# Kernel tuning notes

Hardware: AMD Instinct MI355X
Metric: run time of the kernel (lower is better)

Reference implementation:

```python
import jax, jax.numpy as jnp
import numpy as np


def setup_inputs() -> dict:
    key = jax.random.key(0)
    k1, k2 = jax.random.split(key)
    embed1 = jax.random.normal(k1, (4096, 32), dtype=jnp.float32)
    embed2 = jax.random.normal(k2, (4096, 32), dtype=jnp.float32)
    return {"embed1": embed1, "embed2": embed2}


def reference(embed1, embed2):
    # Chebyshev (L-inf) pairwise distance matrix: [N, M]
    # diff: [N, M, D] broadcasted subtract, abs, max over feature dim D
    return jnp.max(jnp.abs(embed1[:, None, :] - embed2[None, :, :]), axis=2)
```

## Files before the change

### kernel.cpp

```cpp
#include <hip/hip_runtime.h>

#define FD 32
#define TILE 64
#define LSTRIDE (TILE + 4)

__global__ __launch_bounds__(256) void cheb_kernel(
    const float* __restrict__ A, const float* __restrict__ B,
    float* __restrict__ C, int N, int M)
{
    __shared__ float sA[FD][LSTRIDE];
    __shared__ float sB[FD][LSTRIDE];

    const int tid = threadIdx.x;
    const int r0 = blockIdx.y * TILE;
    const int c0 = blockIdx.x * TILE;

#pragma unroll
    for (int k = 0; k < 2; ++k) {
        const int idx = tid + k * 256;
        const int row = idx >> 3;
        const int dq  = (idx & 7) * 4;
        const float4 va = *reinterpret_cast<const float4*>(A + (size_t)(r0 + row) * FD + dq);
        sA[dq + 0][row] = va.x;
        sA[dq + 1][row] = va.y;
        sA[dq + 2][row] = va.z;
        sA[dq + 3][row] = va.w;
        const float4 vb = *reinterpret_cast<const float4*>(B + (size_t)(c0 + row) * FD + dq);
        sB[dq + 0][row] = vb.x;
        sB[dq + 1][row] = vb.y;
        sB[dq + 2][row] = vb.z;
        sB[dq + 3][row] = vb.w;
    }
    __syncthreads();

    const int tx = tid & 15;
    const int ty = tid >> 4;

    float acc[4][4];
#pragma unroll
    for (int i = 0; i < 4; ++i)
#pragma unroll
        for (int j = 0; j < 4; ++j)
            acc[i][j] = 0.0f;

#pragma unroll
    for (int d = 0; d < FD; ++d) {
        const float4 a4 = *reinterpret_cast<const float4*>(&sA[d][ty * 4]);
        const float4 b4 = *reinterpret_cast<const float4*>(&sB[d][tx * 4]);
        const float a[4] = {a4.x, a4.y, a4.z, a4.w};
        const float b[4] = {b4.x, b4.y, b4.z, b4.w};
#pragma unroll
        for (int i = 0; i < 4; ++i)
#pragma unroll
            for (int j = 0; j < 4; ++j)
                acc[i][j] = fmaxf(acc[i][j], fabsf(a[i] - b[j]));
    }

#pragma unroll
    for (int i = 0; i < 4; ++i) {
        const int row = r0 + ty * 4 + i;
        float4 o;
        o.x = acc[i][0]; o.y = acc[i][1]; o.z = acc[i][2]; o.w = acc[i][3];
        *reinterpret_cast<float4*>(C + (size_t)row * M + c0 + tx * 4) = o;
    }
}

extern "C" void kernel_launch(void* const* d_in, const int* in_sizes, int n_in,
                              void* d_out, int out_size, void* d_ws, size_t ws_size,
                              hipStream_t stream) {
    const float* A = (const float*)d_in[0];
    const float* B = (const float*)d_in[1];
    float* C = (float*)d_out;
    const int N = in_sizes[0] / FD;
    const int M = in_sizes[1] / FD;
    dim3 grid(M / TILE, N / TILE);
    cheb_kernel<<<grid, 256, 0, stream>>>(A, B, C, N, M);
}
```

Before: 25.15 us.

## Use 128x128 tiles with 8x8 per-thread outputs, packed subtract and max3-abs

The block tile grows from 64x64 to 128x128, and each thread now computes an 8x8 block of outputs. Shared memory holds B negated in a paired-dimension layout with an XOR swizzle, so v_pk_add_f32 computes two dimension differences per instruction. v_max3_f32 with abs modifiers then folds both into the running max, roughly halving the VALU instruction count per output. The cost is much higher register pressure (64 accumulators plus operands) and a grid reduced to 1024 blocks, which may lower occupancy.

Measured after the change: 34.76 us. +38.2%, slower.

```diff
diff --git a/kernel.cpp b/kernel.cpp
--- a/kernel.cpp
+++ b/kernel.cpp
@@ -1,67 +1,102 @@
 #include <hip/hip_runtime.h>
 
 #define FD 32
-#define TILE 64
-#define LSTRIDE (TILE + 4)
+#define NDD 16
+#define TILE 128
+#define PLANE 260
+
+__device__ __forceinline__ float2 pk_add(float2 a, float2 b) {
+    float2 r;
+    asm("v_pk_add_f32 %0, %1, %2" : "=v"(r) : "v"(a), "v"(b));
+    return r;
+}
+__device__ __forceinline__ float max3abs(float a, float x, float y) {
+    float r;
+    asm("v_max3_f32 %0, %1, abs(%2), abs(%3)" : "=v"(r) : "v"(a), "v"(x), "v"(y));
+    return r;
+}
 
 __global__ __launch_bounds__(256) void cheb_kernel(
     const float* __restrict__ A, const float* __restrict__ B,
-    float* __restrict__ C, int N, int M)
+    float* __restrict__ C, int M)
 {
-    __shared__ float sA[FD][LSTRIDE];
-    __shared__ float sB[FD][LSTRIDE];
+    __shared__ __align__(16) float sA[NDD * PLANE];
+    __shared__ __align__(16) float sB[NDD * PLANE];
 
     const int tid = threadIdx.x;
     const int r0 = blockIdx.y * TILE;
     const int c0 = blockIdx.x * TILE;
 
 #pragma unroll
-    for (int k = 0; k < 2; ++k) {
+    for (int k = 0; k < 4; ++k) {
         const int idx = tid + k * 256;
         const int row = idx >> 3;
         const int dq  = (idx & 7) * 4;
+        const int c   = row >> 1;
+        const int pc  = c ^ (c >> 3);
+        const int base = (dq >> 1) * PLANE + pc * 4 + (row & 1) * 2;
         const float4 va = *reinterpret_cast<const float4*>(A + (size_t)(r0 + row) * FD + dq);
-        sA[dq + 0][row] = va.x;
-        sA[dq + 1][row] = va.y;
-        sA[dq + 2][row] = va.z;
-        sA[dq + 3][row] = va.w;
+        sA[base + 0] = va.x;  sA[base + 1] = va.y;
+        sA[base + PLANE + 0] = va.z;  sA[base + PLANE + 1] = va.w;
         const float4 vb = *reinterpret_cast<const float4*>(B + (size_t)(c0 + row) * FD + dq);
-        sB[dq + 0][row] = vb.x;
-        sB[dq + 1][row] = vb.y;
-        sB[dq + 2][row] = vb.z;
-        sB[dq + 3][row] = vb.w;
+        sB[base + 0] = -vb.x;  sB[base + 1] = -vb.y;
+        sB[base + PLANE + 0] = -vb.z;  sB[base + PLANE + 1] = -vb.w;
     }
     __syncthreads();
 
     const int tx = tid & 15;
     const int ty = tid >> 4;
 
-    float acc[4][4];
+    float acc[8][8];
 #pragma unroll
-    for (int i = 0; i < 4; ++i)
+    for (int i = 0; i < 8; ++i)
 #pragma unroll
-        for (int j = 0; j < 4; ++j)
+        for (int j = 0; j < 8; ++j)
             acc[i][j] = 0.0f;
 
+    int swA[4], swB[4];
 #pragma unroll
-    for (int d = 0; d < FD; ++d) {
-        const float4 a4 = *reinterpret_cast<const float4*>(&sA[d][ty * 4]);
-        const float4 b4 = *reinterpret_cast<const float4*>(&sB[d][tx * 4]);
-        const float a[4] = {a4.x, a4.y, a4.z, a4.w};
-        const float b[4] = {b4.x, b4.y, b4.z, b4.w};
-#pragma unroll
-        for (int i = 0; i < 4; ++i)
-#pragma unroll
-            for (int j = 0; j < 4; ++j)
-                acc[i][j] = fmaxf(acc[i][j], fabsf(a[i] - b[j]));
+    for (int k = 0; k < 4; ++k) {
+        const int cA = ty * 4 + k;
+        swA[k] = (cA ^ (cA >> 3)) * 4;
+        const int cB = ((k & 2) ? 32 : 0) + 2 * tx + (k & 1);
+        swB[k] = (cB ^ (cB >> 3)) * 4;
     }
 
 #pragma unroll
-    for (int i = 0; i < 4; ++i) {
-        const int row = r0 + ty * 4 + i;
-        float4 o;
-        o.x = acc[i][0]; o.y = acc[i][1]; o.z = acc[i][2]; o.w = acc[i][3];
-        *reinterpret_cast<float4*>(C + (size_t)row * M + c0 + tx * 4) = o;
+    for (int dd = 0; dd < NDD; ++dd) {
+        const float* pA = sA + dd * PLANE;
+        const float* pB = sB + dd * PLANE;
+        float2 pa[8], pb[8];
+#pragma unroll
+        for (int k = 0; k < 4; ++k) {
+            const float4 v = *reinterpret_cast<const float4*>(pA + swA[k]);
+            pa[2 * k]     = make_float2(v.x, v.y);
+            pa[2 * k + 1] = make_float2(v.z, v.w);
+        }
+#pragma unroll
+        for (int k = 0; k < 4; ++k) {
+            const float4 v = *reinterpret_cast<const float4*>(pB + swB[k]);
+            pb[2 * k]     = make_float2(v.x, v.y);
+            pb[2 * k + 1] = make_float2(v.z, v.w);
+        }
+#pragma unroll
+        for (int i = 0; i < 8; ++i)
+#pragma unroll
+            for (int j = 0; j < 8; ++j) {
+                const float2 d2 = pk_add(pa[i], pb[j]);
+                acc[i][j] = max3abs(acc[i][j], d2.x, d2.y);
+            }
+    }
+
+#pragma unroll
+    for (int i = 0; i < 8; ++i) {
+        const size_t rowoff = (size_t)(r0 + ty * 8 + i) * M;
+        float4 o0, o1;
+        o0.x = acc[i][0]; o0.y = acc[i][1]; o0.z = acc[i][2]; o0.w = acc[i][3];
+        o1.x = acc[i][4]; o1.y = acc[i][5]; o1.z = acc[i][6]; o1.w = acc[i][7];
+        *reinterpret_cast<float4*>(C + rowoff + c0 + tx * 4) = o0;
+        *reinterpret_cast<float4*>(C + rowoff + c0 + 64 + tx * 4) = o1;
     }
 }
 
@@ -74,5 +109,5 @@
     const int N = in_sizes[0] / FD;
     const int M = in_sizes[1] / FD;
     dim3 grid(M / TILE, N / TILE);
-    cheb_kernel<<<grid, 256, 0, stream>>>(A, B, C, N, M);
+    cheb_kernel<<<grid, 256, 0, stream>>>(A, B, C, M);
 }
```
